# Kernel optimization log

Hardware: AMD Instinct MI355X
Metric: run time of the kernel (lower is better)

Reference implementation:

```python
import jax, jax.numpy as jnp
import numpy as np

B, S, D = 2, 2048, 2048
H, HD, RD = 16, 128, 64
ND = HD - RD  # nope head dim = 64
QR, KVR = 1536, 512  # q/kv lora ranks
EPS = 1e-6


def rmsnorm(x, w):
    return x * jax.lax.rsqrt(jnp.mean(x * x, axis=-1, keepdims=True) + EPS) * w


def rope_rotate(x, cos, sin):
    # x: [B, h, S, r]; cos/sin: [S, r/2]; pairwise complex rotation
    xr, xi = x[..., 0::2], x[..., 1::2]
    o_r = xr * cos - xi * sin
    o_i = xr * sin + xi * cos
    return jnp.stack([o_r, o_i], axis=-1).reshape(x.shape)


def setup_inputs() -> dict:
    key = jax.random.key(0)
    ks = jax.random.split(key, 12)
    sd = 0.02
    # rotary tables for rope_head_dim
    inv_freq = 1.0 / (10000.0 ** (np.arange(0, RD, 2, dtype=np.float32) / RD))
    t = np.arange(S, dtype=np.float32)
    ang = np.outer(t, inv_freq)  # [S, RD/2]
    return {
        "x": jax.random.normal(ks[0], (B, S, D), dtype=jnp.float32),
        "freqs_cos": jnp.asarray(np.cos(ang)),
        "freqs_sin": jnp.asarray(np.sin(ang)),
        "w_cq": jax.random.normal(ks[1], (QR, D), dtype=jnp.float32) * sd,
        "w_dq_nope": jax.random.normal(ks[2], (H * ND, QR), dtype=jnp.float32) * sd,
        "w_dq_rope": jax.random.normal(ks[3], (H * RD, QR), dtype=jnp.float32) * sd,
        "w_ckv": jax.random.normal(ks[4], (KVR, D), dtype=jnp.float32) * sd,
        "w_dk_nope": jax.random.normal(ks[5], (H * ND, KVR), dtype=jnp.float32) * sd,
        "w_dv": jax.random.normal(ks[6], (H * HD, KVR), dtype=jnp.float32) * sd,
        "w_krope": jax.random.normal(ks[7], (RD, D), dtype=jnp.float32) * sd,
        "w_proj": jax.random.normal(ks[8], (H * HD, H * HD), dtype=jnp.float32) * sd,
        "q_norm_w": jnp.ones((QR,), dtype=jnp.float32),
        "kv_norm_w": jnp.ones((KVR,), dtype=jnp.float32),
    }


def reference(x, freqs_cos, freqs_sin, w_cq, w_dq_nope, w_dq_rope, w_ckv,
              w_dk_nope, w_dv, w_krope, w_proj, q_norm_w, kv_norm_w):
    b, s, _ = x.shape
    # low-rank q path
    norm_q = rmsnorm(jnp.einsum("bsd,rd->bsr", x, w_cq), q_norm_w)
    q_nope = jnp.einsum("bsr,or->bso", norm_q, w_dq_nope).reshape(b, s, H, ND).transpose(0, 2, 1, 3)
    q_rope = jnp.einsum("bsr,or->bso", norm_q, w_dq_rope).reshape(b, s, H, RD).transpose(0, 2, 1, 3)
    # low-rank kv path
    norm_kv = rmsnorm(jnp.einsum("bsd,rd->bsr", x, w_ckv), kv_norm_w)
    k_nope = jnp.einsum("bsr,or->bso", norm_kv, w_dk_nope).reshape(b, s, H, ND).transpose(0, 2, 1, 3)
    v = jnp.einsum("bsr,or->bso", norm_kv, w_dv).reshape(b, s, H, HD).transpose(0, 2, 1, 3)
    # shared single-head rope key from x directly
    k_rope_raw = jnp.einsum("bsd,rd->bsr", x, w_krope).reshape(b, s, 1, RD).transpose(0, 2, 1, 3)
    # NOTE: source does `k_rope, q_rope = apply_rope(query_rope, key_rope, cis)`,
    # i.e. the rotated query lands in the K slot and the rotated (1-head) key in the Q slot.
    k_rope = rope_rotate(q_rope, freqs_cos, freqs_sin)            # [B,H,S,RD]
    q_rope_out = rope_rotate(k_rope_raw, freqs_cos, freqs_sin)     # [B,1,S,RD]
    q = jnp.concatenate([q_nope, jnp.broadcast_to(q_rope_out, (b, H, s, RD))], axis=-1)
    k = jnp.concatenate([k_nope, k_rope], axis=-1)
    # causal SDPA, scale 1/sqrt(head_dim)
    scores = jnp.einsum("bhqd,bhkd->bhqk", q, k) / jnp.sqrt(jnp.float32(HD))
    mask = jnp.tril(jnp.ones((s, s), dtype=bool))
    scores = jnp.where(mask, scores, jnp.finfo(scores.dtype).min)
    attn = jax.nn.softmax(scores, axis=-1)
    out = jnp.einsum("bhqk,bhkd->bhqd", attn, v)  # [B,H,S,HD]
    out = out.transpose(0, 2, 1, 3).reshape(b, s, H * HD)
    return jnp.einsum("bso,po->bsp", out, w_proj)
```

## Files before the change

### kernel.cpp

```cpp
#include <hip/hip_runtime.h>

typedef __attribute__((ext_vector_type(4))) float f32x4;
typedef __attribute__((ext_vector_type(8))) short short8;
typedef unsigned short ushort_t;

__device__ __forceinline__ float bf2f(ushort_t u) {
  unsigned int i = ((unsigned int)u) << 16;
  return __builtin_bit_cast(float, i);
}
__device__ __forceinline__ ushort_t f2bf(float f) {
  unsigned int x = __builtin_bit_cast(unsigned int, f);
  unsigned int r = (x + 0x7FFFu + ((x >> 16) & 1u)) >> 16;
  return (ushort_t)r;
}

__global__ __launch_bounds__(256)
void cvt_all(const float* __restrict__ x, const float* __restrict__ wcq,
             const float* __restrict__ wdqn, const float* __restrict__ wdqr,
             const float* __restrict__ wckv, const float* __restrict__ wdkn,
             const float* __restrict__ wdv, const float* __restrict__ wkr,
             const float* __restrict__ wpr,
             ushort_t* ox, ushort_t* owcq, ushort_t* owdqn, ushort_t* owdqr,
             ushort_t* owckv, ushort_t* owdkn, ushort_t* owdv, ushort_t* owkr,
             ushort_t* owpr) {
  int bid = blockIdx.x;
  const float* in; ushort_t* out;
  if (bid < 8192)       { in = x;    out = ox;    }
  else if (bid < 11264) { in = wcq;  out = owcq;  bid -= 8192;  }
  else if (bid < 12800) { in = wdqn; out = owdqn; bid -= 11264; }
  else if (bid < 14336) { in = wdqr; out = owdqr; bid -= 12800; }
  else if (bid < 15360) { in = wckv; out = owckv; bid -= 14336; }
  else if (bid < 15872) { in = wdkn; out = owdkn; bid -= 15360; }
  else if (bid < 16896) { in = wdv;  out = owdv;  bid -= 15872; }
  else if (bid < 17024) { in = wkr;  out = owkr;  bid -= 16896; }
  else                  { in = wpr;  out = owpr;  bid -= 17024; }
  const long i = ((long)bid * 256 + threadIdx.x) * 4;
  float4 v = *(const float4*)(in + i);
  ushort4 o;
  o.x = f2bf(v.x); o.y = f2bf(v.y); o.z = f2bf(v.z); o.w = f2bf(v.w);
  *(ushort4*)(out + i) = o;
}

template <int OUT_BF16>
__global__ __launch_bounds__(256)
void gemm_bt(const ushort_t* __restrict__ A, const ushort_t* __restrict__ B,
             void* __restrict__ Cv, int M, int N, int K) {
  __shared__ __align__(16) ushort_t As[128 * 64];
  __shared__ __align__(16) ushort_t Bs[128 * 64];
  const int tid = threadIdx.x;
  const int lane = tid & 63;
  const int wid = tid >> 6;
  const int m0 = blockIdx.y * 128;
  const int n0 = blockIdx.x * 128;
  const int wm = (wid >> 1) * 64;
  const int wn = (wid & 1) * 64;

  f32x4 acc[4][4];
#pragma unroll
  for (int m = 0; m < 4; ++m)
#pragma unroll
    for (int n = 0; n < 4; ++n) acc[m][n] = (f32x4){0.f, 0.f, 0.f, 0.f};

  const int ktiles = K >> 6;
  for (int kt = 0; kt < ktiles; ++kt) {
    const int k0 = kt << 6;
    __syncthreads();
#pragma unroll
    for (int i = 0; i < 4; ++i) {
      const int chunk = (i * 4 + wid) * 1024;
      const int o = chunk + lane * 16;
      const int row = o >> 7;
      const int cb = o & 127;
      const ushort_t* src = A + (long)(m0 + row) * K + (k0 + (cb >> 1));
      __builtin_amdgcn_global_load_lds((const __attribute__((address_space(1))) unsigned int*)src,
                                       (__attribute__((address_space(3))) unsigned int*)((char*)As + chunk),
                                       16, 0, 0);
    }
#pragma unroll
    for (int i = 0; i < 4; ++i) {
      const int chunk = (i * 4 + wid) * 1024;
      const int o = chunk + lane * 16;
      const int row = o >> 7;
      const int cb = o & 127;
      int brow = n0 + row;
      if (brow > N - 1) brow = N - 1;
      const ushort_t* src = B + (long)brow * K + (k0 + (cb >> 1));
      __builtin_amdgcn_global_load_lds((const __attribute__((address_space(1))) unsigned int*)src,
                                       (__attribute__((address_space(3))) unsigned int*)((char*)Bs + chunk),
                                       16, 0, 0);
    }
    __syncthreads();
#pragma unroll
    for (int kk = 0; kk < 2; ++kk) {
      const int kb = kk * 32 + ((lane >> 4) << 3);
      short8 a[4], b[4];
#pragma unroll
      for (int m = 0; m < 4; ++m)
        a[m] = *(const short8*)(As + (wm + m * 16 + (lane & 15)) * 64 + kb);
#pragma unroll
      for (int n = 0; n < 4; ++n)
        b[n] = *(const short8*)(Bs + (wn + n * 16 + (lane & 15)) * 64 + kb);
#pragma unroll
      for (int m = 0; m < 4; ++m)
#pragma unroll
        for (int n = 0; n < 4; ++n)
          acc[m][n] = __builtin_amdgcn_mfma_f32_16x16x32_bf16(a[m], b[n], acc[m][n], 0, 0, 0);
    }
  }
  const int rb = m0 + wm + ((lane >> 4) << 2);
  const int cbase = n0 + wn + (lane & 15);
#pragma unroll
  for (int m = 0; m < 4; ++m)
#pragma unroll
    for (int n = 0; n < 4; ++n) {
      const int c = cbase + n * 16;
      if (c < N) {
#pragma unroll
        for (int j = 0; j < 4; ++j) {
          const long r = rb + m * 16 + j;
          if (OUT_BF16)
            ((ushort_t*)Cv)[r * N + c] = f2bf(acc[m][n][j]);
          else
            ((float*)Cv)[r * N + c] = acc[m][n][j];
        }
      }
    }
}

__global__ __launch_bounds__(256)
void gemm_bt3(const ushort_t* __restrict__ A,
              const ushort_t* __restrict__ B0, ushort_t* __restrict__ C0, int nb0, int N0,
              const ushort_t* __restrict__ B1, ushort_t* __restrict__ C1, int nb1, int N1,
              const ushort_t* __restrict__ B2, ushort_t* __restrict__ C2, int N2,
              int K) {
  __shared__ __align__(16) ushort_t As[128 * 64];
  __shared__ __align__(16) ushort_t Bs[128 * 64];
  int bx = blockIdx.x;
  const ushort_t* Bp; ushort_t* Cp; int N;
  if (bx < nb0)            { Bp = B0; Cp = C0; N = N0; }
  else if (bx < nb0 + nb1) { Bp = B1; Cp = C1; N = N1; bx -= nb0; }
  else                     { Bp = B2; Cp = C2; N = N2; bx -= nb0 + nb1; }
  const int tid = threadIdx.x;
  const int lane = tid & 63;
  const int wid = tid >> 6;
  const int m0 = blockIdx.y * 128;
  const int n0 = bx * 128;
  const int wm = (wid >> 1) * 64;
  const int wn = (wid & 1) * 64;

  f32x4 acc[4][4];
#pragma unroll
  for (int m = 0; m < 4; ++m)
#pragma unroll
    for (int n = 0; n < 4; ++n) acc[m][n] = (f32x4){0.f, 0.f, 0.f, 0.f};

  const int ktiles = K >> 6;
  for (int kt = 0; kt < ktiles; ++kt) {
    const int k0 = kt << 6;
    __syncthreads();
#pragma unroll
    for (int i = 0; i < 4; ++i) {
      const int chunk = (i * 4 + wid) * 1024;
      const int o = chunk + lane * 16;
      const int row = o >> 7;
      const int cb = o & 127;
      const ushort_t* src = A + (long)(m0 + row) * K + (k0 + (cb >> 1));
      __builtin_amdgcn_global_load_lds((const __attribute__((address_space(1))) unsigned int*)src,
                                       (__attribute__((address_space(3))) unsigned int*)((char*)As + chunk),
                                       16, 0, 0);
    }
#pragma unroll
    for (int i = 0; i < 4; ++i) {
      const int chunk = (i * 4 + wid) * 1024;
      const int o = chunk + lane * 16;
      const int row = o >> 7;
      const int cb = o & 127;
      int brow = n0 + row;
      if (brow > N - 1) brow = N - 1;
      const ushort_t* src = Bp + (long)brow * K + (k0 + (cb >> 1));
      __builtin_amdgcn_global_load_lds((const __attribute__((address_space(1))) unsigned int*)src,
                                       (__attribute__((address_space(3))) unsigned int*)((char*)Bs + chunk),
                                       16, 0, 0);
    }
    __syncthreads();
#pragma unroll
    for (int kk = 0; kk < 2; ++kk) {
      const int kb = kk * 32 + ((lane >> 4) << 3);
      short8 a[4], b[4];
#pragma unroll
      for (int m = 0; m < 4; ++m)
        a[m] = *(const short8*)(As + (wm + m * 16 + (lane & 15)) * 64 + kb);
#pragma unroll
      for (int n = 0; n < 4; ++n)
        b[n] = *(const short8*)(Bs + (wn + n * 16 + (lane & 15)) * 64 + kb);
#pragma unroll
      for (int m = 0; m < 4; ++m)
#pragma unroll
        for (int n = 0; n < 4; ++n)
          acc[m][n] = __builtin_amdgcn_mfma_f32_16x16x32_bf16(a[m], b[n], acc[m][n], 0, 0, 0);
    }
  }
  const int rb = m0 + wm + ((lane >> 4) << 2);
  const int cbase = n0 + wn + (lane & 15);
#pragma unroll
  for (int m = 0; m < 4; ++m)
#pragma unroll
    for (int n = 0; n < 4; ++n) {
      const int c = cbase + n * 16;
      if (c < N) {
#pragma unroll
        for (int j = 0; j < 4; ++j) {
          const long r = rb + m * 16 + j;
          Cp[r * N + c] = f2bf(acc[m][n][j]);
        }
      }
    }
}

__device__ __forceinline__ void rms_body(const ushort_t* x, const float* w,
                                         ushort_t* out, int R, float* warr) {
  const int tid = threadIdx.x;
  float ss = 0.f;
  for (int i = tid; i < R; i += 256) { float v = bf2f(x[i]); ss += v * v; }
#pragma unroll
  for (int off = 32; off; off >>= 1) ss += __shfl_xor(ss, off);
  if ((tid & 63) == 0) warr[tid >> 6] = ss;
  __syncthreads();
  const float tot = warr[0] + warr[1] + warr[2] + warr[3];
  const float rs = rsqrtf(tot / (float)R + 1e-6f);
  for (int i = tid; i < R; i += 256) out[i] = f2bf(bf2f(x[i]) * rs * w[i]);
}

__global__ __launch_bounds__(256)
void rmsnorm_both(const ushort_t* __restrict__ ckv, const float* __restrict__ kvnw,
                  ushort_t* __restrict__ nkv,
                  const ushort_t* __restrict__ cq, const float* __restrict__ qnw,
                  ushort_t* __restrict__ nq) {
  __shared__ float warr[4];
  const int bid = blockIdx.x;
  if (bid < 4096) rms_body(ckv + (long)bid * 512, kvnw, nkv + (long)bid * 512, 512, warr);
  else {
    const long row = bid - 4096;
    rms_body(cq + row * 1536, qnw, nq + row * 1536, 1536, warr);
  }
}

__device__ __forceinline__ void rope_body(const ushort_t* in, ushort_t* out,
                                          const float* fc, const float* fs,
                                          int heads, int bid) {
  const int idx = bid * 256 + threadIdx.x;
  const int i = idx & 31;
  const int rest = idx >> 5;
  const int hh = rest % heads;
  const int row = rest / heads;
  const int srow = row & 2047;
  const float c = fc[srow * 32 + i];
  const float s = fs[srow * 32 + i];
  const long base = (long)row * heads * 64 + hh * 64 + 2 * i;
  const float x0 = bf2f(in[base]);
  const float x1 = bf2f(in[base + 1]);
  out[base] = f2bf(x0 * c - x1 * s);
  out[base + 1] = f2bf(x0 * s + x1 * c);
}

__global__ __launch_bounds__(256)
void rope_kraw(const ushort_t* __restrict__ kraw, ushort_t* __restrict__ qrs,
               const float* __restrict__ fc, const float* __restrict__ fs) {
  rope_body(kraw, qrs, fc, fs, 1, blockIdx.x);
}

__global__ __launch_bounds__(256)
void tv_rope(const ushort_t* __restrict__ v, ushort_t* __restrict__ vt,
             const ushort_t* __restrict__ qr, ushort_t* __restrict__ krope,
             const float* __restrict__ fc, const float* __restrict__ fs) {
  __shared__ __align__(16) ushort_t Ts[64 * 128];
  const int bid = blockIdx.x;
  if (bid >= 1024) { rope_body(qr, krope, fc, fs, 16, bid - 1024); return; }
  const int t = threadIdx.x;
  const int bh = bid >> 5;
  const int b = bh >> 4, h = bh & 15;
  const int s0 = (bid & 31) * 64;
#pragma unroll
  for (int i = 0; i < 4; ++i) {
    const int c = t + 256 * i;
    const int si = c >> 4;
    const int xb = (c & 15) * 16;
    const long src = ((long)b * 2048 + s0 + si) * 2048 + h * 128 + (xb >> 1);
    short8 val = *(const short8*)(v + src);
    *(short8*)((char*)Ts + si * 256 + (xb ^ ((si & 15) << 4))) = val;
  }
  __syncthreads();
  const int d = (t & 63) + ((t >> 7) << 6);
  const int scb = ((t >> 6) & 1) * 4;
#pragma unroll
  for (int i = 0; i < 4; ++i) {
    const int sc = scb + i;
    short8 val;
#pragma unroll
    for (int j = 0; j < 8; ++j) {
      const int s = sc * 8 + j;
      val[j] = (short)*(const ushort_t*)((const char*)Ts + s * 256 + ((2 * d) ^ ((s & 15) << 4)));
    }
    *(short8*)(vt + ((long)bh * 128 + d) * 2048 + s0 + sc * 8) = val;
  }
}

__global__ __launch_bounds__(512)
void attn_mfma(const ushort_t* __restrict__ qn, const ushort_t* __restrict__ qrs,
               const ushort_t* __restrict__ kn, const ushort_t* __restrict__ kr,
               const ushort_t* __restrict__ vt, ushort_t* __restrict__ out) {
  __shared__ __align__(16) ushort_t Ks[2][8192];
  __shared__ __align__(16) ushort_t Vts[2][8192];
  __shared__ __align__(16) ushort_t Ps[16384];
  const int tid = threadIdx.x, lane = tid & 63, wid = tid >> 6;
  const int g = lane >> 4, lq = lane & 15;
  const int bh = blockIdx.x, b = bh >> 4, h = bh & 15;
  const float scale = 0.08838834764831845f;
  char* Pbase = (char*)Ps + wid * 2048;

  auto stageK = [&](int bsel, int kt) {
    const int k0s = kt * 64;
#pragma unroll
    for (int i = 0; i < 2; ++i) {
      const int cc = wid * 2 + i;
      const int o = cc * 1024 + lane * 16;
      const int row = o >> 8;
      const int dK = ((o & 255) ^ ((row & 7) << 4)) >> 1;
      const long krow = (long)b * 2048 + k0s + row;
      const ushort_t* srcK = (dK < 64) ? (kn + krow * 1024 + h * 64 + dK)
                                       : (kr + krow * 1024 + h * 64 + (dK - 64));
      __builtin_amdgcn_global_load_lds((const __attribute__((address_space(1))) unsigned int*)srcK,
          (__attribute__((address_space(3))) unsigned int*)((char*)Ks[bsel] + cc * 1024), 16, 0, 0);
    }
  };
  auto stageV = [&](int bsel, int kt) {
    const int k0s = kt * 64;
#pragma unroll
    for (int i = 0; i < 2; ++i) {
      const int cc = wid * 2 + i;
      const int o = cc * 1024 + lane * 16;
      const int dr = o >> 7;
      const int se = ((o & 127) ^ ((dr & 7) << 4)) >> 1;
      const ushort_t* srcV = vt + ((long)bh * 128 + dr) * 2048 + k0s + se;
      __builtin_amdgcn_global_load_lds((const __attribute__((address_space(1))) unsigned int*)srcV,
          (__attribute__((address_space(3))) unsigned int*)((char*)Vts[bsel] + cc * 1024), 16, 0, 0);
    }
  };

  const int pair = blockIdx.y;
  for (int half = 0; half < 2; ++half) {
    const int tq = half ? (15 - pair) : pair;
    const int q0 = tq * 128;
    const int qw0 = q0 + wid * 16;
    short8 aq[4];
    {
      const long grow = (long)b * 2048 + qw0 + lq;
#pragma unroll
      for (int ks = 0; ks < 4; ++ks) {
        const int d = ks * 32 + g * 8;
        const ushort_t* src = (d < 64) ? (qn + grow * 1024 + h * 64 + d)
                                       : (qrs + grow * 64 + (d - 64));
        aq[ks] = *(const short8*)src;
      }
    }
    f32x4 oacc[8];
#pragma unroll
    for (int n = 0; n < 8; ++n) oacc[n] = (f32x4){0.f, 0.f, 0.f, 0.f};
    float sm[4] = {-3e38f, -3e38f, -3e38f, -3e38f};
    float sl[4] = {0.f, 0.f, 0.f, 0.f};

    auto qk = [&](f32x4 (&sacc)[4], int u) {
#pragma unroll
      for (int n = 0; n < 4; ++n) sacc[n] = (f32x4){0.f, 0.f, 0.f, 0.f};
      const ushort_t* Kbuf = Ks[u & 1];
      __builtin_amdgcn_s_setprio(1);
#pragma unroll
      for (int ks = 0; ks < 4; ++ks) {
        const int x = ks * 64 + g * 16;
#pragma unroll
        for (int n = 0; n < 4; ++n) {
          const int kl = n * 16 + lq;
          short8 bk = *(const short8*)((const char*)Kbuf + kl * 256 + (x ^ ((kl & 7) << 4)));
          sacc[n] = __builtin_amdgcn_mfma_f32_16x16x32_bf16(aq[ks], bk, sacc[n], 0, 0, 0);
        }
      }
      __builtin_amdgcn_s_setprio(0);
    };
    auto process = [&](f32x4 (&sacc)[4], int u) {
      const int k0 = u * 64;
      if (k0 + 63 > qw0) {
#pragma unroll
        for (int n = 0; n < 4; ++n) {
          const int key = k0 + n * 16 + lq;
#pragma unroll
          for (int j = 0; j < 4; ++j) {
            const int qrow = qw0 + g * 4 + j;
            if (key > qrow) sacc[n][j] = -3e38f;
          }
        }
      }
      float tmax[4];
#pragma unroll
      for (int j = 0; j < 4; ++j)
        tmax[j] = fmaxf(fmaxf(sacc[0][j], sacc[1][j]), fmaxf(sacc[2][j], sacc[3][j]));
#pragma unroll
      for (int off = 1; off < 16; off <<= 1)
#pragma unroll
        for (int j = 0; j < 4; ++j) tmax[j] = fmaxf(tmax[j], __shfl_xor(tmax[j], off));
      bool need = false;
#pragma unroll
      for (int j = 0; j < 4; ++j) {
        tmax[j] *= scale;
        need = need || (tmax[j] > sm[j] + 8.f);
      }
      if (__any(need)) {
#pragma unroll
        for (int j = 0; j < 4; ++j) {
          const float mn = fmaxf(sm[j], tmax[j]);
          const float fr = __expf(sm[j] - mn);
          sm[j] = mn;
          sl[j] *= fr;
#pragma unroll
          for (int n = 0; n < 8; ++n) oacc[n][j] *= fr;
        }
      }
      f32x4 p[4];
#pragma unroll
      for (int n = 0; n < 4; ++n)
#pragma unroll
        for (int j = 0; j < 4; ++j)
          p[n][j] = __expf(__builtin_fmaf(sacc[n][j], scale, -sm[j]));
      float psum[4];
#pragma unroll
      for (int j = 0; j < 4; ++j) psum[j] = p[0][j] + p[1][j] + p[2][j] + p[3][j];
#pragma unroll
      for (int off = 1; off < 16; off <<= 1)
#pragma unroll
        for (int j = 0; j < 4; ++j) psum[j] += __shfl_xor(psum[j], off);
#pragma unroll
      for (int j = 0; j < 4; ++j) sl[j] += psum[j];
#pragma unroll
      for (int n = 0; n < 4; ++n) {
        const int col2 = (n * 16 + lq) * 2;
#pragma unroll
        for (int j = 0; j < 4; ++j) {
          const int row = g * 4 + j;
          *(ushort_t*)(Pbase + row * 128 + (col2 ^ ((row & 7) << 4))) = f2bf(p[n][j]);
        }
      }
      const ushort_t* Vbuf = Vts[u & 1];
      __builtin_amdgcn_s_setprio(1);
#pragma unroll
      for (int ks2 = 0; ks2 < 2; ++ks2) {
        const int x = ks2 * 64 + g * 16;
        short8 pa = *(const short8*)(Pbase + lq * 128 + (x ^ ((lq & 7) << 4)));
#pragma unroll
        for (int nd = 0; nd < 8; ++nd) {
          const int dl = nd * 16 + lq;
          short8 vb = *(const short8*)((const char*)Vbuf + dl * 128 + (x ^ ((dl & 7) << 4)));
          oacc[nd] = __builtin_amdgcn_mfma_f32_16x16x32_bf16(pa, vb, oacc[nd], 0, 0, 0);
        }
      }
      __builtin_amdgcn_s_setprio(0);
    };

    const int kmax = 2 * tq + 2;
    f32x4 saccA[4], saccB[4];
    stageK(0, 0); stageV(0, 0); stageK(1, 1);
    asm volatile("s_waitcnt vmcnt(0)" ::: "memory");
    __builtin_amdgcn_s_barrier();
    __builtin_amdgcn_sched_barrier(0);
    qk(saccA, 0);
    for (int u = 0; u < kmax; u += 2) {
      if (u + 2 < kmax) stageK(0, u + 2);
      stageV(1, u + 1);
      qk(saccB, u + 1);
      process(saccA, u);
      asm volatile("s_waitcnt vmcnt(0)" ::: "memory");
      __builtin_amdgcn_s_barrier();
      __builtin_amdgcn_sched_barrier(0);
      if (u + 3 < kmax) stageK(1, u + 3);
      if (u + 2 < kmax) stageV(0, u + 2);
      if (u + 2 < kmax) qk(saccA, u + 2);
      process(saccB, u + 1);
      asm volatile("s_waitcnt vmcnt(0)" ::: "memory");
      __builtin_amdgcn_s_barrier();
      __builtin_amdgcn_sched_barrier(0);
    }
    float inv[4];
#pragma unroll
    for (int j = 0; j < 4; ++j) inv[j] = 1.f / sl[j];
#pragma unroll
    for (int nd = 0; nd < 8; ++nd) {
      const int d = nd * 16 + lq;
#pragma unroll
      for (int j = 0; j < 4; ++j) {
        const long row = (long)b * 2048 + qw0 + g * 4 + j;
        out[row * 2048 + h * 128 + d] = f2bf(oacc[nd][j] * inv[j]);
      }
    }
  }
}

extern "C" void kernel_launch(void* const* d_in, const int* in_sizes, int n_in,
                              void* d_out, int out_size, void* d_ws, size_t ws_size,
                              hipStream_t stream) {
  const float* x      = (const float*)d_in[0];
  const float* fcos   = (const float*)d_in[1];
  const float* fsin   = (const float*)d_in[2];
  const float* w_cq   = (const float*)d_in[3];
  const float* w_dqn  = (const float*)d_in[4];
  const float* w_dqr  = (const float*)d_in[5];
  const float* w_ckv  = (const float*)d_in[6];
  const float* w_dkn  = (const float*)d_in[7];
  const float* w_dv   = (const float*)d_in[8];
  const float* w_kr   = (const float*)d_in[9];
  const float* w_proj = (const float*)d_in[10];
  const float* qnw    = (const float*)d_in[11];
  const float* kvnw   = (const float*)d_in[12];
  float* out = (float*)d_out;

  char* ws = (char*)d_ws;
  ushort_t* x_bf     = (ushort_t*)(ws + 0);
  ushort_t* wcq_bf   = (ushort_t*)(ws + 16777216);
  ushort_t* wdqn_bf  = (ushort_t*)(ws + 23068672);
  ushort_t* wdqr_bf  = (ushort_t*)(ws + 26214400);
  ushort_t* wckv_bf  = (ushort_t*)(ws + 29360128);
  ushort_t* wdkn_bf  = (ushort_t*)(ws + 31457280);
  ushort_t* wdv_bf   = (ushort_t*)(ws + 32505856);
  ushort_t* wpr_bf   = (ushort_t*)(ws + 34603008);
  ushort_t* cq_bf    = (ushort_t*)(ws + 42991616);
  ushort_t* krope_bf = (ushort_t*)(ws + 42991616);
  ushort_t* qrs_bf   = (ushort_t*)(ws + 51904512);
  ushort_t* ckv_bf   = (ushort_t*)(ws + 55574528);
  ushort_t* nq_bf    = (ushort_t*)(ws + 59768832);
  ushort_t* attn_bf  = (ushort_t*)(ws + 55574528);
  ushort_t* nkv_bf   = (ushort_t*)(ws + 72351744);
  ushort_t* qnope_bf = (ushort_t*)(ws + 76546048);
  ushort_t* kraw_bf  = (ushort_t*)(ws + 76546048);
  ushort_t* qr_bf    = (ushort_t*)(ws + 0);
  ushort_t* knope_bf = (ushort_t*)(ws + 8388608);
  ushort_t* v_bf     = (ushort_t*)(ws + 84934656);
  ushort_t* wkr_bf   = (ushort_t*)(ws + 84934656);
  ushort_t* vt_bf    = (ushort_t*)(ws + 16777216);

  cvt_all<<<21120, 256, 0, stream>>>(x, w_cq, w_dqn, w_dqr, w_ckv, w_dkn, w_dv, w_kr, w_proj,
                                     x_bf, wcq_bf, wdqn_bf, wdqr_bf, wckv_bf, wdkn_bf,
                                     wdv_bf, wkr_bf, wpr_bf);
  gemm_bt3<<<dim3(17, 32), 256, 0, stream>>>(x_bf,
                                             wckv_bf, ckv_bf, 4, 512,
                                             wcq_bf, cq_bf, 12, 1536,
                                             wkr_bf, kraw_bf, 64, 2048);
  rmsnorm_both<<<8192, 256, 0, stream>>>(ckv_bf, kvnw, nkv_bf, cq_bf, qnw, nq_bf);
  rope_kraw<<<512, 256, 0, stream>>>(kraw_bf, qrs_bf, fcos, fsin);
  gemm_bt3<<<dim3(16, 32), 256, 0, stream>>>(nq_bf,
                                             wdqn_bf, qnope_bf, 8, 1024,
                                             wdqr_bf, qr_bf, 8, 1024,
                                             wdqn_bf, qnope_bf, 1024, 1536);
  gemm_bt3<<<dim3(24, 32), 256, 0, stream>>>(nkv_bf,
                                             wdkn_bf, knope_bf, 8, 1024,
                                             wdv_bf, v_bf, 16, 2048,
                                             wdkn_bf, knope_bf, 1024, 512);
  tv_rope<<<9216, 256, 0, stream>>>(v_bf, vt_bf, qr_bf, krope_bf, fcos, fsin);
  attn_mfma<<<dim3(32, 8), 512, 0, stream>>>(qnope_bf, qrs_bf, knope_bf, krope_bf, vt_bf, attn_bf);
  gemm_bt<0><<<dim3(16, 32), 256, 0, stream>>>(attn_bf, wpr_bf, out, 4096, 2048, 2048);
}
```

Baseline: 341.0 us.

## Fuse V transpose into GEMM epilogue and split attention q-tiles across blocks

The V-projection GEMM now writes its output tile through shared memory transposed directly into the Vt layout, so the separate transpose pass and the intermediate V buffer are no longer needed. The leftover rope work becomes its own small kernel. Attention now launches one block per query tile (grid y 16) instead of pairing two tiles per block, and the P scratch buffer is halved. This doubles block-level parallelism for attention, but per-block work is now imbalanced, with heavy tiles launched first.

```diff
diff --git a/kernel.cpp b/kernel.cpp
--- a/kernel.cpp
+++ b/kernel.cpp
@@ -132,14 +132,15 @@
               const ushort_t* __restrict__ B0, ushort_t* __restrict__ C0, int nb0, int N0,
               const ushort_t* __restrict__ B1, ushort_t* __restrict__ C1, int nb1, int N1,
               const ushort_t* __restrict__ B2, ushort_t* __restrict__ C2, int N2,
-              int K) {
-  __shared__ __align__(16) ushort_t As[128 * 64];
-  __shared__ __align__(16) ushort_t Bs[128 * 64];
+              int K, int tvSeg) {
+  __shared__ __align__(16) ushort_t S[16384];
+  ushort_t* As = S;
+  ushort_t* Bs = S + 8192;
   int bx = blockIdx.x;
-  const ushort_t* Bp; ushort_t* Cp; int N;
-  if (bx < nb0)            { Bp = B0; Cp = C0; N = N0; }
-  else if (bx < nb0 + nb1) { Bp = B1; Cp = C1; N = N1; bx -= nb0; }
-  else                     { Bp = B2; Cp = C2; N = N2; bx -= nb0 + nb1; }
+  const ushort_t* Bp; ushort_t* Cp; int N; int seg;
+  if (bx < nb0)            { Bp = B0; Cp = C0; N = N0; seg = 0; }
+  else if (bx < nb0 + nb1) { Bp = B1; Cp = C1; N = N1; seg = 1; bx -= nb0; }
+  else                     { Bp = B2; Cp = C2; N = N2; seg = 2; bx -= nb0 + nb1; }
   const int tid = threadIdx.x;
   const int lane = tid & 63;
   const int wid = tid >> 6;
@@ -199,6 +200,40 @@
         for (int n = 0; n < 4; ++n)
           acc[m][n] = __builtin_amdgcn_mfma_f32_16x16x32_bf16(a[m], b[n], acc[m][n], 0, 0, 0);
     }
+  }
+  if (seg == tvSeg) {
+    __syncthreads();
+    const int lrb = wm + ((lane >> 4) << 2);
+    const int ldb = wn + (lane & 15);
+#pragma unroll
+    for (int m = 0; m < 4; ++m)
+#pragma unroll
+      for (int n = 0; n < 4; ++n) {
+        const int ld = ldb + n * 16;
+#pragma unroll
+        for (int j = 0; j < 4; ++j) {
+          const int lr = lrb + m * 16 + j;
+          *(ushort_t*)((char*)S + lr * 256 + ((2 * ld) ^ ((lr & 15) << 4))) = f2bf(acc[m][n][j]);
+        }
+      }
+    __syncthreads();
+    const int b = m0 >> 11;
+    const int s0 = m0 & 2047;
+    const int bh = b * 16 + bx;
+    const int d = tid & 127;
+    const int sh = (tid >> 7) * 64;
+#pragma unroll
+    for (int i = 0; i < 8; ++i) {
+      const int sbase = sh + i * 8;
+      short8 val;
+#pragma unroll
+      for (int j = 0; j < 8; ++j) {
+        const int s = sbase + j;
+        val[j] = (short)*(const ushort_t*)((const char*)S + s * 256 + ((2 * d) ^ ((s & 15) << 4)));
+      }
+      *(short8*)(Cp + ((long)bh * 128 + d) * 2048 + s0 + sbase) = val;
+    }
+    return;
   }
   const int rb = m0 + wm + ((lane >> 4) << 2);
   const int cbase = n0 + wn + (lane & 15);
@@ -270,39 +305,9 @@
 }
 
 __global__ __launch_bounds__(256)
-void tv_rope(const ushort_t* __restrict__ v, ushort_t* __restrict__ vt,
-             const ushort_t* __restrict__ qr, ushort_t* __restrict__ krope,
+void rope_qr(const ushort_t* __restrict__ qr, ushort_t* __restrict__ krope,
              const float* __restrict__ fc, const float* __restrict__ fs) {
-  __shared__ __align__(16) ushort_t Ts[64 * 128];
-  const int bid = blockIdx.x;
-  if (bid >= 1024) { rope_body(qr, krope, fc, fs, 16, bid - 1024); return; }
-  const int t = threadIdx.x;
-  const int bh = bid >> 5;
-  const int b = bh >> 4, h = bh & 15;
-  const int s0 = (bid & 31) * 64;
-#pragma unroll
-  for (int i = 0; i < 4; ++i) {
-    const int c = t + 256 * i;
-    const int si = c >> 4;
-    const int xb = (c & 15) * 16;
-    const long src = ((long)b * 2048 + s0 + si) * 2048 + h * 128 + (xb >> 1);
-    short8 val = *(const short8*)(v + src);
-    *(short8*)((char*)Ts + si * 256 + (xb ^ ((si & 15) << 4))) = val;
-  }
-  __syncthreads();
-  const int d = (t & 63) + ((t >> 7) << 6);
-  const int scb = ((t >> 6) & 1) * 4;
-#pragma unroll
-  for (int i = 0; i < 4; ++i) {
-    const int sc = scb + i;
-    short8 val;
-#pragma unroll
-    for (int j = 0; j < 8; ++j) {
-      const int s = sc * 8 + j;
-      val[j] = (short)*(const ushort_t*)((const char*)Ts + s * 256 + ((2 * d) ^ ((s & 15) << 4)));
-    }
-    *(short8*)(vt + ((long)bh * 128 + d) * 2048 + s0 + sc * 8) = val;
-  }
+  rope_body(qr, krope, fc, fs, 16, blockIdx.x);
 }
 
 __global__ __launch_bounds__(512)
@@ -311,7 +316,7 @@
                const ushort_t* __restrict__ vt, ushort_t* __restrict__ out) {
   __shared__ __align__(16) ushort_t Ks[2][8192];
   __shared__ __align__(16) ushort_t Vts[2][8192];
-  __shared__ __align__(16) ushort_t Ps[16384];
+  __shared__ __align__(16) ushort_t Ps[8192];
   const int tid = threadIdx.x, lane = tid & 63, wid = tid >> 6;
   const int g = lane >> 4, lq = lane & 15;
   const int bh = blockIdx.x, b = bh >> 4, h = bh & 15;
@@ -347,157 +352,155 @@
     }
   };
 
-  const int pair = blockIdx.y;
-  for (int half = 0; half < 2; ++half) {
-    const int tq = half ? (15 - pair) : pair;
-    const int q0 = tq * 128;
-    const int qw0 = q0 + wid * 16;
-    short8 aq[4];
-    {
-      const long grow = (long)b * 2048 + qw0 + lq;
-#pragma unroll
-      for (int ks = 0; ks < 4; ++ks) {
-        const int d = ks * 32 + g * 8;
-        const ushort_t* src = (d < 64) ? (qn + grow * 1024 + h * 64 + d)
-                                       : (qrs + grow * 64 + (d - 64));
-        aq[ks] = *(const short8*)src;
-      }
-    }
-    f32x4 oacc[8];
-#pragma unroll
-    for (int n = 0; n < 8; ++n) oacc[n] = (f32x4){0.f, 0.f, 0.f, 0.f};
-    float sm[4] = {-3e38f, -3e38f, -3e38f, -3e38f};
-    float sl[4] = {0.f, 0.f, 0.f, 0.f};
-
-    auto qk = [&](f32x4 (&sacc)[4], int u) {
-#pragma unroll
-      for (int n = 0; n < 4; ++n) sacc[n] = (f32x4){0.f, 0.f, 0.f, 0.f};
-      const ushort_t* Kbuf = Ks[u & 1];
-      __builtin_amdgcn_s_setprio(1);
-#pragma unroll
-      for (int ks = 0; ks < 4; ++ks) {
-        const int x = ks * 64 + g * 16;
-#pragma unroll
-        for (int n = 0; n < 4; ++n) {
-          const int kl = n * 16 + lq;
-          short8 bk = *(const short8*)((const char*)Kbuf + kl * 256 + (x ^ ((kl & 7) << 4)));
-          sacc[n] = __builtin_amdgcn_mfma_f32_16x16x32_bf16(aq[ks], bk, sacc[n], 0, 0, 0);
+  const int y = blockIdx.y;
+  const int tq = (y < 8) ? (15 - y) : (y - 8);
+  const int q0 = tq * 128;
+  const int qw0 = q0 + wid * 16;
+  short8 aq[4];
+  {
+    const long grow = (long)b * 2048 + qw0 + lq;
+#pragma unroll
+    for (int ks = 0; ks < 4; ++ks) {
+      const int d = ks * 32 + g * 8;
+      const ushort_t* src = (d < 64) ? (qn + grow * 1024 + h * 64 + d)
+                                     : (qrs + grow * 64 + (d - 64));
+      aq[ks] = *(const short8*)src;
+    }
+  }
+  f32x4 oacc[8];
+#pragma unroll
+  for (int n = 0; n < 8; ++n) oacc[n] = (f32x4){0.f, 0.f, 0.f, 0.f};
+  float sm[4] = {-3e38f, -3e38f, -3e38f, -3e38f};
+  float sl[4] = {0.f, 0.f, 0.f, 0.f};
+
+  auto qk = [&](f32x4 (&sacc)[4], int u) {
+#pragma unroll
+    for (int n = 0; n < 4; ++n) sacc[n] = (f32x4){0.f, 0.f, 0.f, 0.f};
+    const ushort_t* Kbuf = Ks[u & 1];
+    __builtin_amdgcn_s_setprio(1);
+#pragma unroll
+    for (int ks = 0; ks < 4; ++ks) {
+      const int x = ks * 64 + g * 16;
+#pragma unroll
+      for (int n = 0; n < 4; ++n) {
+        const int kl = n * 16 + lq;
+        short8 bk = *(const short8*)((const char*)Kbuf + kl * 256 + (x ^ ((kl & 7) << 4)));
+        sacc[n] = __builtin_amdgcn_mfma_f32_16x16x32_bf16(aq[ks], bk, sacc[n], 0, 0, 0);
+      }
+    }
+    __builtin_amdgcn_s_setprio(0);
+  };
+  auto process = [&](f32x4 (&sacc)[4], int u) {
+    const int k0 = u * 64;
+    if (k0 + 63 > qw0) {
+#pragma unroll
+      for (int n = 0; n < 4; ++n) {
+        const int key = k0 + n * 16 + lq;
+#pragma unroll
+        for (int j = 0; j < 4; ++j) {
+          const int qrow = qw0 + g * 4 + j;
+          if (key > qrow) sacc[n][j] = -3e38f;
         }
       }
-      __builtin_amdgcn_s_setprio(0);
-    };
-    auto process = [&](f32x4 (&sacc)[4], int u) {
-      const int k0 = u * 64;
-      if (k0 + 63 > qw0) {
-#pragma unroll
-        for (int n = 0; n < 4; ++n) {
-          const int key = k0 + n * 16 + lq;
-#pragma unroll
-          for (int j = 0; j < 4; ++j) {
-            const int qrow = qw0 + g * 4 + j;
-            if (key > qrow) sacc[n][j] = -3e38f;
-          }
-        }
-      }
-      float tmax[4];
+    }
+    float tmax[4];
+#pragma unroll
+    for (int j = 0; j < 4; ++j)
+      tmax[j] = fmaxf(fmaxf(sacc[0][j], sacc[1][j]), fmaxf(sacc[2][j], sacc[3][j]));
+#pragma unroll
+    for (int off = 1; off < 16; off <<= 1)
+#pragma unroll
+      for (int j = 0; j < 4; ++j) tmax[j] = fmaxf(tmax[j], __shfl_xor(tmax[j], off));
+    bool need = false;
+#pragma unroll
+    for (int j = 0; j < 4; ++j) {
+      tmax[j] *= scale;
+      need = need || (tmax[j] > sm[j] + 8.f);
+    }
+    if (__any(need)) {
+#pragma unroll
+      for (int j = 0; j < 4; ++j) {
+        const float mn = fmaxf(sm[j], tmax[j]);
+        const float fr = __expf(sm[j] - mn);
+        sm[j] = mn;
+        sl[j] *= fr;
+#pragma unroll
+        for (int n = 0; n < 8; ++n) oacc[n][j] *= fr;
+      }
+    }
+    f32x4 p[4];
+#pragma unroll
+    for (int n = 0; n < 4; ++n)
 #pragma unroll
       for (int j = 0; j < 4; ++j)
-        tmax[j] = fmaxf(fmaxf(sacc[0][j], sacc[1][j]), fmaxf(sacc[2][j], sacc[3][j]));
-#pragma unroll
-      for (int off = 1; off < 16; off <<= 1)
-#pragma unroll
-        for (int j = 0; j < 4; ++j) tmax[j] = fmaxf(tmax[j], __shfl_xor(tmax[j], off));
-      bool need = false;
+        p[n][j] = __expf(__builtin_fmaf(sacc[n][j], scale, -sm[j]));
+    float psum[4];
+#pragma unroll
+    for (int j = 0; j < 4; ++j) psum[j] = p[0][j] + p[1][j] + p[2][j] + p[3][j];
+#pragma unroll
+    for (int off = 1; off < 16; off <<= 1)
+#pragma unroll
+      for (int j = 0; j < 4; ++j) psum[j] += __shfl_xor(psum[j], off);
+#pragma unroll
+    for (int j = 0; j < 4; ++j) sl[j] += psum[j];
+#pragma unroll
+    for (int n = 0; n < 4; ++n) {
+      const int col2 = (n * 16 + lq) * 2;
 #pragma unroll
       for (int j = 0; j < 4; ++j) {
-        tmax[j] *= scale;
-        need = need || (tmax[j] > sm[j] + 8.f);
-      }
-      if (__any(need)) {
-#pragma unroll
-        for (int j = 0; j < 4; ++j) {
-          const float mn = fmaxf(sm[j], tmax[j]);
-          const float fr = __expf(sm[j] - mn);
-          sm[j] = mn;
-          sl[j] *= fr;
-#pragma unroll
-          for (int n = 0; n < 8; ++n) oacc[n][j] *= fr;
-        }
-      }
-      f32x4 p[4];
-#pragma unroll
-      for (int n = 0; n < 4; ++n)
-#pragma unroll
-        for (int j = 0; j < 4; ++j)
-          p[n][j] = __expf(__builtin_fmaf(sacc[n][j], scale, -sm[j]));
-      float psum[4];
-#pragma unroll
-      for (int j = 0; j < 4; ++j) psum[j] = p[0][j] + p[1][j] + p[2][j] + p[3][j];
-#pragma unroll
-      for (int off = 1; off < 16; off <<= 1)
-#pragma unroll
-        for (int j = 0; j < 4; ++j) psum[j] += __shfl_xor(psum[j], off);
-#pragma unroll
-      for (int j = 0; j < 4; ++j) sl[j] += psum[j];
-#pragma unroll
-      for (int n = 0; n < 4; ++n) {
-        const int col2 = (n * 16 + lq) * 2;
-#pragma unroll
-        for (int j = 0; j < 4; ++j) {
-          const int row = g * 4 + j;
-          *(ushort_t*)(Pbase + row * 128 + (col2 ^ ((row & 7) << 4))) = f2bf(p[n][j]);
-        }
-      }
-      const ushort_t* Vbuf = Vts[u & 1];
-      __builtin_amdgcn_s_setprio(1);
-#pragma unroll
-      for (int ks2 = 0; ks2 < 2; ++ks2) {
-        const int x = ks2 * 64 + g * 16;
-        short8 pa = *(const short8*)(Pbase + lq * 128 + (x ^ ((lq & 7) << 4)));
-#pragma unroll
-        for (int nd = 0; nd < 8; ++nd) {
-          const int dl = nd * 16 + lq;
-          short8 vb = *(const short8*)((const char*)Vbuf + dl * 128 + (x ^ ((dl & 7) << 4)));
-          oacc[nd] = __builtin_amdgcn_mfma_f32_16x16x32_bf16(pa, vb, oacc[nd], 0, 0, 0);
-        }
-      }
-      __builtin_amdgcn_s_setprio(0);
-    };
-
-    const int kmax = 2 * tq + 2;
-    f32x4 saccA[4], saccB[4];
-    stageK(0, 0); stageV(0, 0); stageK(1, 1);
+        const int row = g * 4 + j;
+        *(ushort_t*)(Pbase + row * 128 + (col2 ^ ((row & 7) << 4))) = f2bf(p[n][j]);
+      }
+    }
+    const ushort_t* Vbuf = Vts[u & 1];
+    __builtin_amdgcn_s_setprio(1);
+#pragma unroll
+    for (int ks2 = 0; ks2 < 2; ++ks2) {
+      const int x = ks2 * 64 + g * 16;
+      short8 pa = *(const short8*)(Pbase + lq * 128 + (x ^ ((lq & 7) << 4)));
+#pragma unroll
+      for (int nd = 0; nd < 8; ++nd) {
+        const int dl = nd * 16 + lq;
+        short8 vb = *(const short8*)((const char*)Vbuf + dl * 128 + (x ^ ((dl & 7) << 4)));
+        oacc[nd] = __builtin_amdgcn_mfma_f32_16x16x32_bf16(pa, vb, oacc[nd], 0, 0, 0);
+      }
+    }
+    __builtin_amdgcn_s_setprio(0);
+  };
+
+  const int kmax = 2 * tq + 2;
+  f32x4 saccA[4], saccB[4];
+  stageK(0, 0); stageV(0, 0); stageK(1, 1);
+  asm volatile("s_waitcnt vmcnt(0)" ::: "memory");
+  __builtin_amdgcn_s_barrier();
+  __builtin_amdgcn_sched_barrier(0);
+  qk(saccA, 0);
+  for (int u = 0; u < kmax; u += 2) {
+    if (u + 2 < kmax) stageK(0, u + 2);
+    stageV(1, u + 1);
+    qk(saccB, u + 1);
+    process(saccA, u);
     asm volatile("s_waitcnt vmcnt(0)" ::: "memory");
     __builtin_amdgcn_s_barrier();
     __builtin_amdgcn_sched_barrier(0);
-    qk(saccA, 0);
-    for (int u = 0; u < kmax; u += 2) {
-      if (u + 2 < kmax) stageK(0, u + 2);
-      stageV(1, u + 1);
-      qk(saccB, u + 1);
-      process(saccA, u);
-      asm volatile("s_waitcnt vmcnt(0)" ::: "memory");
-      __builtin_amdgcn_s_barrier();
-      __builtin_amdgcn_sched_barrier(0);
-      if (u + 3 < kmax) stageK(1, u + 3);
-      if (u + 2 < kmax) stageV(0, u + 2);
-      if (u + 2 < kmax) qk(saccA, u + 2);
-      process(saccB, u + 1);
-      asm volatile("s_waitcnt vmcnt(0)" ::: "memory");
-      __builtin_amdgcn_s_barrier();
-      __builtin_amdgcn_sched_barrier(0);
-    }
-    float inv[4];
-#pragma unroll
-    for (int j = 0; j < 4; ++j) inv[j] = 1.f / sl[j];
-#pragma unroll
-    for (int nd = 0; nd < 8; ++nd) {
-      const int d = nd * 16 + lq;
-#pragma unroll
-      for (int j = 0; j < 4; ++j) {
-        const long row = (long)b * 2048 + qw0 + g * 4 + j;
-        out[row * 2048 + h * 128 + d] = f2bf(oacc[nd][j] * inv[j]);
-      }
+    if (u + 3 < kmax) stageK(1, u + 3);
+    if (u + 2 < kmax) stageV(0, u + 2);
+    if (u + 2 < kmax) qk(saccA, u + 2);
+    process(saccB, u + 1);
+    asm volatile("s_waitcnt vmcnt(0)" ::: "memory");
+    __builtin_amdgcn_s_barrier();
+    __builtin_amdgcn_sched_barrier(0);
+  }
+  float inv[4];
+#pragma unroll
+  for (int j = 0; j < 4; ++j) inv[j] = 1.f / sl[j];
+#pragma unroll
+  for (int nd = 0; nd < 8; ++nd) {
+    const int d = nd * 16 + lq;
+#pragma unroll
+    for (int j = 0; j < 4; ++j) {
+      const long row = (long)b * 2048 + qw0 + g * 4 + j;
+      out[row * 2048 + h * 128 + d] = f2bf(oacc[nd][j] * inv[j]);
     }
   }
 }
@@ -540,9 +543,8 @@
   ushort_t* kraw_bf  = (ushort_t*)(ws + 76546048);
   ushort_t* qr_bf    = (ushort_t*)(ws + 0);
   ushort_t* knope_bf = (ushort_t*)(ws + 8388608);
-  ushort_t* v_bf     = (ushort_t*)(ws + 84934656);
   ushort_t* wkr_bf   = (ushort_t*)(ws + 84934656);
-  ushort_t* vt_bf    = (ushort_t*)(ws + 16777216);
+  ushort_t* vt_bf    = (ushort_t*)(ws + 84934656);
 
   cvt_all<<<21120, 256, 0, stream>>>(x, w_cq, w_dqn, w_dqr, w_ckv, w_dkn, w_dv, w_kr, w_proj,
                                      x_bf, wcq_bf, wdqn_bf, wdqr_bf, wckv_bf, wdkn_bf,
@@ -550,18 +552,18 @@
   gemm_bt3<<<dim3(17, 32), 256, 0, stream>>>(x_bf,
                                              wckv_bf, ckv_bf, 4, 512,
                                              wcq_bf, cq_bf, 12, 1536,
-                                             wkr_bf, kraw_bf, 64, 2048);
+                                             wkr_bf, kraw_bf, 64, 2048, -1);
   rmsnorm_both<<<8192, 256, 0, stream>>>(ckv_bf, kvnw, nkv_bf, cq_bf, qnw, nq_bf);
   rope_kraw<<<512, 256, 0, stream>>>(kraw_bf, qrs_bf, fcos, fsin);
   gemm_bt3<<<dim3(16, 32), 256, 0, stream>>>(nq_bf,
                                              wdqn_bf, qnope_bf, 8, 1024,
                                              wdqr_bf, qr_bf, 8, 1024,
-                                             wdqn_bf, qnope_bf, 1024, 1536);
+                                             wdqn_bf, qnope_bf, 1024, 1536, -1);
   gemm_bt3<<<dim3(24, 32), 256, 0, stream>>>(nkv_bf,
                                              wdkn_bf, knope_bf, 8, 1024,
-                                             wdv_bf, v_bf, 16, 2048,
-                                             wdkn_bf, knope_bf, 1024, 512);
-  tv_rope<<<9216, 256, 0, stream>>>(v_bf, vt_bf, qr_bf, krope_bf, fcos, fsin);
-  attn_mfma<<<dim3(32, 8), 512, 0, stream>>>(qnope_bf, qrs_bf, knope_bf, krope_bf, vt_bf, attn_bf);
+                                             wdv_bf, vt_bf, 16, 2048,
+                                             wdkn_bf, knope_bf, 1024, 512, 1);
+  rope_qr<<<8192, 256, 0, stream>>>(qr_bf, krope_bf, fcos, fsin);
+  attn_mfma<<<dim3(32, 16), 512, 0, stream>>>(qnope_bf, qrs_bf, knope_bf, krope_bf, vt_bf, attn_bf);
   gemm_bt<0><<<dim3(16, 32), 256, 0, stream>>>(attn_bf, wpr_bf, out, 4096, 2048, 2048);
 }
```

Result: slower. 360.2 us (+5.7%).
